# Optimization experiments

Measured on AMD Instinct MI355X. Metric: run time of the kernel, lower is better.

## Reference

```python
import jax, jax.numpy as jnp
import numpy as np

STATE_DIM = 512
N_AGENTS = 16
N_ACTIONS = 32
EMBED = 512          # mixing_embed_dim
Q_IN = STATE_DIM + N_AGENTS * N_ACTIONS  # 1024 (coma_critic arch)
ROWS = 32768         # bs * ts = 64 * 512


def _linear_params(key, d_in, d_out):
    kw, kb = jax.random.split(key)
    bound = 1.0 / np.sqrt(d_in)
    W = jax.random.uniform(kw, (d_in, d_out), minval=-bound, maxval=bound, dtype=jnp.float32)
    b = jax.random.uniform(kb, (d_out,), minval=-bound, maxval=bound, dtype=jnp.float32)
    return W, b


def setup_inputs() -> dict:
    key = jax.random.key(0)
    ks = jax.random.split(key, 8)
    states = jax.random.normal(ks[0], (ROWS, STATE_DIM), dtype=jnp.float32)
    actions = jax.random.uniform(ks[1], (ROWS, N_AGENTS * N_ACTIONS), dtype=jnp.float32)
    Qw1, Qb1 = _linear_params(ks[2], Q_IN, EMBED)
    Qw2, Qb2 = _linear_params(ks[3], EMBED, EMBED)
    Qw3, Qb3 = _linear_params(ks[4], EMBED, 1)
    Vw1, Vb1 = _linear_params(ks[5], STATE_DIM, EMBED)
    Vw2, Vb2 = _linear_params(ks[6], EMBED, EMBED)
    Vw3, Vb3 = _linear_params(ks[7], EMBED, 1)
    return {
        "states": states, "actions": actions,
        "Qw1": Qw1, "Qb1": Qb1, "Qw2": Qw2, "Qb2": Qb2, "Qw3": Qw3, "Qb3": Qb3,
        "Vw1": Vw1, "Vb1": Vb1, "Vw2": Vw2, "Vb2": Vb2, "Vw3": Vw3, "Vb3": Vb3,
    }


def _mlp3(x, W1, b1, W2, b2, W3, b3):
    h = jax.nn.relu(x @ W1 + b1)
    h = jax.nn.relu(h @ W2 + b2)
    return h @ W3 + b3


def reference(states, actions,
              Qw1, Qb1, Qw2, Qb2, Qw3, Qb3,
              Vw1, Vb1, Vw2, Vb2, Vw3, Vb3):
    # coma_critic arch: inputs = cat([states, joint-action one-hots], dim=1)
    inputs = jnp.concatenate([states, actions], axis=1)  # [bs*ts, Q_IN]
    q_outputs = _mlp3(inputs, Qw1, Qb1, Qw2, Qb2, Qw3, Qb3)  # [bs*ts, 1]
    v_outputs = _mlp3(states, Vw1, Vb1, Vw2, Vb2, Vw3, Vb3)  # [bs*ts, 1]
    return q_outputs, v_outputs
```

## Files before the change

kernel.cpp:

```cpp
#include <hip/hip_runtime.h>


#define ROWS 32768
#define EMBED 512

using frag_ab = __attribute__((ext_vector_type(8))) short;
using f32x4   = __attribute__((ext_vector_type(4))) float;

__device__ __forceinline__ unsigned short f2bf(float f) {
    unsigned int u = __builtin_bit_cast(unsigned int, f);
    return (unsigned short)((u + 0x7fffu + ((u >> 16) & 1u)) >> 16);
}

__device__ __forceinline__ unsigned pk2rne(float lo, float hi) {
    return (unsigned)f2bf(lo) | ((unsigned)f2bf(hi) << 16);
}

__device__ __forceinline__ void async_copy16(const void* g, void* l) {
    __builtin_amdgcn_global_load_lds(
        (const __attribute__((address_space(1))) unsigned int*)g,
        (__attribute__((address_space(3))) unsigned int*)l, 16, 0, 0);
}

#define VM8()   asm volatile("s_waitcnt vmcnt(8)" ::: "memory")
#define VM0()   asm volatile("s_waitcnt vmcnt(0)" ::: "memory")
#define SBAR()  __builtin_amdgcn_s_barrier()

__global__ __launch_bounds__(256)
void prep(const float* __restrict__ states, const float* __restrict__ actions,
          const float* __restrict__ Qw1, const float* __restrict__ Qw2,
          const float* __restrict__ Vw1, const float* __restrict__ Vw2,
          const float* __restrict__ qb3, const float* __restrict__ vb3,
          unsigned short* __restrict__ X,
          unsigned short* __restrict__ Qw1t, unsigned short* __restrict__ Qw2t,
          unsigned short* __restrict__ Vw1t, unsigned short* __restrict__ Vw2t,
          float* __restrict__ out) {
    const int b = blockIdx.x, tid = threadIdx.x;
    if (b < 16384) {
        int g = b * 256 + tid;
        int m = g >> 7, col = (g & 127) * 8;
        const float* src = (col < 512) ? states + (size_t)m * 512 + col
                                       : actions + (size_t)m * 512 + (col - 512);
        float4 f0 = ((const float4*)src)[0];
        float4 f1 = ((const float4*)src)[1];
        *(uint4*)(X + (size_t)m * 1024 + col) =
            make_uint4(pk2rne(f0.x, f0.y), pk2rne(f0.z, f0.w),
                       pk2rne(f1.x, f1.y), pk2rne(f1.z, f1.w));
    } else if (b < 16704) {
        __shared__ float T[64][65];
        int tg = b - 16384;
        const float* W; unsigned short* O; int Krows, kt, nt;
        if (tg < 128) { W = Qw1; O = Qw1t; Krows = 1024; kt = tg >> 3; nt = tg & 7; }
        else {
            tg -= 128; int seg = tg >> 6, r = tg & 63;
            kt = r >> 3; nt = r & 7; Krows = 512;
            W = (seg == 0) ? Qw2 : (seg == 1) ? Vw1 : Vw2;
            O = (seg == 0) ? Qw2t : (seg == 1) ? Vw1t : Vw2t;
        }
        const int k0 = kt * 64, n0 = nt * 64;
        const int rr = tid >> 4, c4 = (tid & 15) * 4;
#pragma unroll
        for (int p = 0; p < 4; ++p) {
            float4 v = *(const float4*)&W[(size_t)(k0 + p * 16 + rr) * 512 + n0 + c4];
            T[p * 16 + rr][c4]     = v.x;
            T[p * 16 + rr][c4 + 1] = v.y;
            T[p * 16 + rr][c4 + 2] = v.z;
            T[p * 16 + rr][c4 + 3] = v.w;
        }
        __syncthreads();
        const int n = tid >> 2, kc = (tid & 3) * 16;
        unsigned pk[8];
#pragma unroll
        for (int j = 0; j < 8; ++j)
            pk[j] = pk2rne(T[kc + 2 * j][n], T[kc + 2 * j + 1][n]);
        uint4* dst = (uint4*)(O + (size_t)(n0 + n) * Krows + k0 + kc);
        dst[0] = make_uint4(pk[0], pk[1], pk[2], pk[3]);
        dst[1] = make_uint4(pk[4], pk[5], pk[6], pk[7]);
    } else {
        int i = (b - 16704) * 256 + tid;
        out[i] = (i < ROWS) ? qb3[0] : vb3[0];
    }
}

__device__ __forceinline__ void gemm_256(
    const unsigned short* __restrict__ A, int ldaE,
    const unsigned short* __restrict__ Bt, int ldbE,
    int K, int bm, int bn, char* smb, f32x4 acc[8][4])
{
    const int tid = threadIdx.x, wave = tid >> 6, lane = tid & 63;
    const int im = wave >> 2, in = wave & 3;
    const int lrow = lane & 15, quad = lane >> 4;
    const int ldaB = ldaE * 2, ldbB = ldbE * 2;

    const int srow = wave * 8 + (lane >> 3);
    const int scol = (((lane & 7) ^ ((lane >> 3) & 7)) << 4);
    const char* gA = (const char*)A + (size_t)(bm + srow) * ldaB + scol;
    const char* gB = (const char*)Bt + (size_t)(bn + srow) * ldbB + scol;
    char* ldsAw = smb + wave * 1024;
    char* ldsBw = smb + 65536 + wave * 1024;

    auto stageTile = [&](int b) {
#pragma unroll
        for (int h = 0; h < 2; ++h) {
            const char* g = gA + (size_t)(h * 128) * ldaB;
            char* l = ldsAw + b * 32768 + h * 16384;
            async_copy16(g, l);
            async_copy16(g + (size_t)64 * ldaB, l + 8192);
        }
#pragma unroll
        for (int h = 0; h < 2; ++h) {
            const char* g = gB + (size_t)(h * 128) * ldbB;
            char* l = ldsBw + b * 32768 + h * 16384;
            async_copy16(g, l);
            async_copy16(g + (size_t)64 * ldbB, l + 8192);
        }
        gA += 128; gB += 128;
    };

    frag_ab a[4][2], b0[2][2], b1[2][2];

    auto readA = [&](int b, int mh) {
        const char* base = smb + b * 32768 + im * 16384;
#pragma unroll
        for (int i = 0; i < 4; ++i) {
            const int r = mh * 64 + i * 16 + lrow;
#pragma unroll
            for (int s = 0; s < 2; ++s)
                a[i][s] = *(const frag_ab*)(base + r * 128 +
                              (((s * 4 + quad) ^ (r & 7)) << 4));
        }
    };
    auto readB = [&](int b, int nh, frag_ab bb[2][2]) {
#pragma unroll
        for (int j = 0; j < 2; ++j) {
            const int nr = in * 64 + nh * 32 + j * 16 + lrow;
            const char* base = smb + 65536 + b * 32768 + (nr >> 7) * 16384;
            const int r = nr & 127;
#pragma unroll
            for (int s = 0; s < 2; ++s)
                bb[j][s] = *(const frag_ab*)(base + r * 128 +
                               (((s * 4 + quad) ^ (r & 7)) << 4));
        }
    };
    auto mma = [&](int mh, int nh, frag_ab bb[2][2]) {
        __builtin_amdgcn_s_setprio(1);
#pragma unroll
        for (int s = 0; s < 2; ++s)
#pragma unroll
            for (int i = 0; i < 4; ++i)
#pragma unroll
                for (int j = 0; j < 2; ++j)
                    acc[mh * 4 + i][nh * 2 + j] =
                        __builtin_amdgcn_mfma_f32_16x16x32_bf16(
                            a[i][s], bb[j][s], acc[mh * 4 + i][nh * 2 + j],
                            0, 0, 0);
        __builtin_amdgcn_s_setprio(0);
    };

    stageTile(0);
    stageTile(1);

    const int NT = K >> 6;
    int buf = 0;
    for (int t = 0; t < NT; ++t) {
        if (t + 1 < NT) VM8(); else VM0();
        SBAR();
        readA(buf, 0); readB(buf, 0, b0);
        mma(0, 0, b0);
        readB(buf, 1, b1);
        mma(0, 1, b1);
        readA(buf, 1);
        mma(1, 1, b1);
        mma(1, 0, b0);
        SBAR();
        if (t + 2 < NT) stageTile(buf);
        buf ^= 1;
    }
}

__device__ __forceinline__ void decode_work(int bid, int& mi, int& v) {
    int work = ((bid & 7) << 6) | (bid >> 3);
    mi = work >> 2; v = work & 3;
}

__global__ __launch_bounds__(512, 2)
void layer1(const unsigned short* __restrict__ X,
            const unsigned short* __restrict__ Qw1t,
            const unsigned short* __restrict__ Vw1t,
            const float* __restrict__ Qb1, const float* __restrict__ Vb1,
            unsigned short* __restrict__ h1Q, unsigned short* __restrict__ h1V) {
    __shared__ __align__(16) char smem[131072];
    int mi, v; decode_work(blockIdx.x, mi, v);
    const bool isV = v >= 2;
    const int bm = mi * 256, bn = (v & 1) * 256;
    const int K = isV ? 512 : 1024;
    const unsigned short* Wt = isV ? Vw1t : Qw1t;
    const float* bias = isV ? Vb1 : Qb1;
    unsigned short* H = isV ? h1V : h1Q;

    f32x4 acc[8][4] = {};
    gemm_256(X, 1024, Wt, K, K, bm, bn, smem, acc);

    const int tid = threadIdx.x, wave = tid >> 6, lane = tid & 63;
    const int im = wave >> 2, in = wave & 3;
    const int lrow = lane & 15, quad = lane >> 4;
#pragma unroll
    for (int j = 0; j < 4; ++j) {
        const int col = bn + in * 64 + j * 16 + lrow;
        const float bc = bias[col];
#pragma unroll
        for (int i = 0; i < 8; ++i) {
            const int row0 = bm + im * 128 + i * 16 + quad * 4;
#pragma unroll
            for (int r = 0; r < 4; ++r) {
                float val = acc[i][j][r] + bc;
                val = val > 0.0f ? val : 0.0f;
                H[(size_t)(row0 + r) * EMBED + col] = f2bf(val);
            }
        }
    }
}

__global__ __launch_bounds__(512, 2)
void layer2(const unsigned short* __restrict__ h1Q,
            const unsigned short* __restrict__ h1V,
            const unsigned short* __restrict__ Qw2t,
            const unsigned short* __restrict__ Vw2t,
            const float* __restrict__ Qb2, const float* __restrict__ Vb2,
            const float* __restrict__ Qw3, const float* __restrict__ Vw3,
            float* __restrict__ out) {
    __shared__ __align__(16) char smem[131072];
    int mi, v; decode_work(blockIdx.x, mi, v);
    const bool isV = v >= 2;
    const int bm = mi * 256, bn = (v & 1) * 256;
    const unsigned short* A  = isV ? h1V : h1Q;
    const unsigned short* Wt = isV ? Vw2t : Qw2t;
    const float* bias = isV ? Vb2 : Qb2;
    const float* w3   = isV ? Vw3 : Qw3;
    float* op = out + (isV ? ROWS : 0);

    f32x4 acc[8][4] = {};
    gemm_256(A, 512, Wt, 512, 512, bm, bn, smem, acc);

    const int tid = threadIdx.x, wave = tid >> 6, lane = tid & 63;
    const int im = wave >> 2, in = wave & 3;
    const int lrow = lane & 15, quad = lane >> 4;
    float bc[4], wc[4];
#pragma unroll
    for (int j = 0; j < 4; ++j) {
        const int col = bn + in * 64 + j * 16 + lrow;
        bc[j] = bias[col];
        wc[j] = w3[col];
    }
#pragma unroll
    for (int i = 0; i < 8; ++i) {
#pragma unroll
        for (int r = 0; r < 4; ++r) {
            float s = 0.0f;
#pragma unroll
            for (int j = 0; j < 4; ++j) {
                float val = acc[i][j][r] + bc[j];
                val = val > 0.0f ? val : 0.0f;
                s += val * wc[j];
            }
#pragma unroll
            for (int m = 1; m < 16; m <<= 1) s += __shfl_xor(s, m, 64);
            if (lrow == 0)
                atomicAdd(&op[bm + im * 128 + i * 16 + quad * 4 + r], s);
        }
    }
}

extern "C" void kernel_launch(void* const* d_in, const int* in_sizes, int n_in,
                              void* d_out, int out_size, void* d_ws, size_t ws_size,
                              hipStream_t stream) {
    const float* states  = (const float*)d_in[0];
    const float* actions = (const float*)d_in[1];
    const float* Qw1 = (const float*)d_in[2];
    const float* Qb1 = (const float*)d_in[3];
    const float* Qw2 = (const float*)d_in[4];
    const float* Qb2 = (const float*)d_in[5];
    const float* Qw3 = (const float*)d_in[6];
    const float* Qb3 = (const float*)d_in[7];
    const float* Vw1 = (const float*)d_in[8];
    const float* Vb1 = (const float*)d_in[9];
    const float* Vw2 = (const float*)d_in[10];
    const float* Vb2 = (const float*)d_in[11];
    const float* Vw3 = (const float*)d_in[12];
    const float* Vb3 = (const float*)d_in[13];
    float* out = (float*)d_out;

    char* ws = (char*)d_ws;
    unsigned short* X    = (unsigned short*)ws;
    unsigned short* h1Q  = (unsigned short*)(ws + 67108864);
    unsigned short* h1V  = (unsigned short*)(ws + 100663296);
    unsigned short* Qw1t = (unsigned short*)(ws + 134217728);
    unsigned short* Qw2t = Qw1t + 512 * 1024;
    unsigned short* Vw1t = Qw2t + 512 * 512;
    unsigned short* Vw2t = Vw1t + 512 * 512;

    prep<<<dim3(16960), dim3(256), 0, stream>>>(states, actions, Qw1, Qw2, Vw1, Vw2,
                                                Qb3, Vb3, X, Qw1t, Qw2t, Vw1t, Vw2t, out);

    layer1<<<dim3(512), dim3(512), 0, stream>>>(X, Qw1t, Vw1t, Qb1, Vb1, h1Q, h1V);
    layer2<<<dim3(512), dim3(512), 0, stream>>>(h1Q, h1V, Qw2t, Vw2t, Qb2, Vb2, Qw3, Vw3, out);
}
```

Measured before the change: 283.0 us.

## Fuse fp32-to-bf16 input conversion into layer1 and merge Q/V work per block

Drops the separate prep pass that converted states/actions to a bf16 X buffer. layer1 now loads fp32 A tiles into registers, converts them to bf16 and writes them to LDS while B tiles stream in asynchronously. Each block handles the Q and V GEMMs for the same row tile back to back, so grids shrink to 256 blocks and the states tile is reread while likely still in cache. This removes a 64MB round-trip through memory, at the cost of register-staged A loads, extra LDS waits and half as many blocks for parallelism.

After: 292.1 us. 1.03x slower.

```diff
diff --git a/kernel.cpp b/kernel.cpp
--- a/kernel.cpp
+++ b/kernel.cpp
@@ -22,33 +22,23 @@
         (__attribute__((address_space(3))) unsigned int*)l, 16, 0, 0);
 }
 
+#define VM12()  asm volatile("s_waitcnt vmcnt(12)" ::: "memory")
 #define VM8()   asm volatile("s_waitcnt vmcnt(8)" ::: "memory")
 #define VM0()   asm volatile("s_waitcnt vmcnt(0)" ::: "memory")
+#define LGKM0() asm volatile("s_waitcnt lgkmcnt(0)" ::: "memory")
 #define SBAR()  __builtin_amdgcn_s_barrier()
 
 __global__ __launch_bounds__(256)
-void prep(const float* __restrict__ states, const float* __restrict__ actions,
-          const float* __restrict__ Qw1, const float* __restrict__ Qw2,
+void prep(const float* __restrict__ Qw1, const float* __restrict__ Qw2,
           const float* __restrict__ Vw1, const float* __restrict__ Vw2,
           const float* __restrict__ qb3, const float* __restrict__ vb3,
-          unsigned short* __restrict__ X,
           unsigned short* __restrict__ Qw1t, unsigned short* __restrict__ Qw2t,
           unsigned short* __restrict__ Vw1t, unsigned short* __restrict__ Vw2t,
           float* __restrict__ out) {
     const int b = blockIdx.x, tid = threadIdx.x;
-    if (b < 16384) {
-        int g = b * 256 + tid;
-        int m = g >> 7, col = (g & 127) * 8;
-        const float* src = (col < 512) ? states + (size_t)m * 512 + col
-                                       : actions + (size_t)m * 512 + (col - 512);
-        float4 f0 = ((const float4*)src)[0];
-        float4 f1 = ((const float4*)src)[1];
-        *(uint4*)(X + (size_t)m * 1024 + col) =
-            make_uint4(pk2rne(f0.x, f0.y), pk2rne(f0.z, f0.w),
-                       pk2rne(f1.x, f1.y), pk2rne(f1.z, f1.w));
-    } else if (b < 16704) {
+    if (b < 320) {
         __shared__ float T[64][65];
-        int tg = b - 16384;
+        int tg = b;
         const float* W; unsigned short* O; int Krows, kt, nt;
         if (tg < 128) { W = Qw1; O = Qw1t; Krows = 1024; kt = tg >> 3; nt = tg & 7; }
         else {
@@ -77,42 +67,198 @@
         dst[0] = make_uint4(pk[0], pk[1], pk[2], pk[3]);
         dst[1] = make_uint4(pk[4], pk[5], pk[6], pk[7]);
     } else {
-        int i = (b - 16704) * 256 + tid;
+        int i = (b - 320) * 256 + tid;
         out[i] = (i < ROWS) ? qb3[0] : vb3[0];
     }
 }
 
+__device__ __forceinline__ void decode_work(int bid, int& mi, int& n) {
+    int work = ((bid & 7) << 5) | (bid >> 3);
+    mi = work >> 1; n = work & 1;
+}
+
+__global__ __launch_bounds__(512, 2)
+void layer1(const float* __restrict__ states, const float* __restrict__ actions,
+            const unsigned short* __restrict__ Qw1t,
+            const unsigned short* __restrict__ Vw1t,
+            const float* __restrict__ Qb1, const float* __restrict__ Vb1,
+            unsigned short* __restrict__ h1Q, unsigned short* __restrict__ h1V) {
+    __shared__ __align__(16) char smem[131072];
+    const int tid = threadIdx.x, wave = tid >> 6, lane = tid & 63;
+    int mi, nh; decode_work(blockIdx.x, mi, nh);
+    const int bm = mi * 256, bn = nh * 256;
+    const int im = wave >> 2, in = wave & 3;
+    const int lrow = lane & 15, quad = lane >> 4;
+
+    const int arow = wave * 8 + (lane >> 3);
+    const int acol = (lane & 7) * 8;
+    const size_t aOff = (size_t)(bm + arow) * 512 + acol;
+
+    const int srow = wave * 8 + (lane >> 3);
+    const int scol = (((lane & 7) ^ ((lane >> 3) & 7)) << 4);
+
+    float4 rA[4][2];
+    frag_ab a[4][2], b0[2][2], b1[2][2];
+    f32x4 acc[8][4] = {};
+
+    auto loadA = [&](const float* p) {
+#pragma unroll
+        for (int q = 0; q < 4; ++q) {
+            const float* s = p + (size_t)(64 * q) * 512;
+            rA[q][0] = *(const float4*)s;
+            rA[q][1] = *(const float4*)(s + 4);
+        }
+    };
+    auto writeA = [&](int b) {
+#pragma unroll
+        for (int q = 0; q < 4; ++q) {
+            const int R = arow + 64 * q, half = R >> 7, r = R & 127;
+            const int c = (lane & 7) ^ (r & 7);
+            *(uint4*)(smem + b * 32768 + half * 16384 + r * 128 + (c << 4)) =
+                make_uint4(pk2rne(rA[q][0].x, rA[q][0].y),
+                           pk2rne(rA[q][0].z, rA[q][0].w),
+                           pk2rne(rA[q][1].x, rA[q][1].y),
+                           pk2rne(rA[q][1].z, rA[q][1].w));
+        }
+    };
+    auto readA = [&](int b, int mh) {
+        const char* base = smem + b * 32768 + im * 16384;
+#pragma unroll
+        for (int i = 0; i < 4; ++i) {
+            const int r = mh * 64 + i * 16 + lrow;
+#pragma unroll
+            for (int s = 0; s < 2; ++s)
+                a[i][s] = *(const frag_ab*)(base + r * 128 +
+                              (((s * 4 + quad) ^ (r & 7)) << 4));
+        }
+    };
+    auto readB = [&](int b, int nhh, frag_ab bb[2][2]) {
+#pragma unroll
+        for (int j = 0; j < 2; ++j) {
+            const int nr = in * 64 + nhh * 32 + j * 16 + lrow;
+            const char* base = smem + 65536 + b * 32768 + (nr >> 7) * 16384;
+            const int r = nr & 127;
+#pragma unroll
+            for (int s = 0; s < 2; ++s)
+                bb[j][s] = *(const frag_ab*)(base + r * 128 +
+                               (((s * 4 + quad) ^ (r & 7)) << 4));
+        }
+    };
+    auto mma = [&](int mh, int nhh, frag_ab bb[2][2]) {
+        __builtin_amdgcn_s_setprio(1);
+#pragma unroll
+        for (int s = 0; s < 2; ++s)
+#pragma unroll
+            for (int i = 0; i < 4; ++i)
+#pragma unroll
+                for (int j = 0; j < 2; ++j)
+                    acc[mh * 4 + i][nhh * 2 + j] =
+                        __builtin_amdgcn_mfma_f32_16x16x32_bf16(
+                            a[i][s], bb[j][s], acc[mh * 4 + i][nhh * 2 + j],
+                            0, 0, 0);
+        __builtin_amdgcn_s_setprio(0);
+    };
+
+    auto run = [&](const float* aP0, const float* aP1, int nt0, int nt1,
+                   const unsigned short* Wt, int ldbE) {
+        const int NT = nt0 + nt1;
+        const int ldbB = ldbE * 2;
+        const char* gB = (const char*)Wt + (size_t)(bn + srow) * ldbB + scol;
+        auto stageB = [&](int b) {
+#pragma unroll
+            for (int h = 0; h < 2; ++h) {
+                const char* g = gB + (size_t)(h * 128) * ldbB;
+                char* l = smem + 65536 + wave * 1024 + b * 32768 + h * 16384;
+                async_copy16(g, l);
+                async_copy16(g + (size_t)64 * ldbB, l + 8192);
+            }
+            gB += 128;
+        };
+        auto aTile = [&](int kt) {
+            return (kt < nt0) ? aP0 + aOff + kt * 64
+                              : aP1 + aOff + (kt - nt0) * 64;
+        };
+        loadA(aTile(0));
+        stageB(0);
+        writeA(0);
+        LGKM0();
+        for (int t = 0; t < NT; ++t) {
+            const bool more = t + 1 < NT;
+            if (more) { loadA(aTile(t + 1)); stageB((t + 1) & 1); }
+            if (more) VM12(); else VM0();
+            SBAR();
+            const int bb = t & 1;
+            readA(bb, 0); readB(bb, 0, b0);
+            mma(0, 0, b0);
+            readB(bb, 1, b1);
+            mma(0, 1, b1);
+            readA(bb, 1);
+            mma(1, 1, b1);
+            mma(1, 0, b0);
+            if (more) writeA((t + 1) & 1);
+            LGKM0();
+            SBAR();
+        }
+    };
+
+    auto epilogue = [&](const float* bias, unsigned short* H) {
+#pragma unroll
+        for (int j = 0; j < 4; ++j) {
+            const int col = bn + in * 64 + j * 16 + lrow;
+            const float bc = bias[col];
+#pragma unroll
+            for (int i = 0; i < 8; ++i) {
+                const int row0 = bm + im * 128 + i * 16 + quad * 4;
+#pragma unroll
+                for (int r = 0; r < 4; ++r) {
+                    float val = acc[i][j][r] + bc;
+                    val = val > 0.0f ? val : 0.0f;
+                    H[(size_t)(row0 + r) * EMBED + col] = f2bf(val);
+                }
+            }
+        }
+    };
+
+    run(states, actions, 8, 8, Qw1t, 1024);
+    epilogue(Qb1, h1Q);
+#pragma unroll
+    for (int i = 0; i < 8; ++i)
+#pragma unroll
+        for (int j = 0; j < 4; ++j) acc[i][j] = f32x4{0.f, 0.f, 0.f, 0.f};
+    run(states, states, 8, 0, Vw1t, 512);
+    epilogue(Vb1, h1V);
+}
+
 __device__ __forceinline__ void gemm_256(
-    const unsigned short* __restrict__ A, int ldaE,
-    const unsigned short* __restrict__ Bt, int ldbE,
-    int K, int bm, int bn, char* smb, f32x4 acc[8][4])
+    const unsigned short* __restrict__ A,
+    const unsigned short* __restrict__ Bt,
+    int bm, int bn, char* smb, f32x4 acc[8][4])
 {
     const int tid = threadIdx.x, wave = tid >> 6, lane = tid & 63;
     const int im = wave >> 2, in = wave & 3;
     const int lrow = lane & 15, quad = lane >> 4;
-    const int ldaB = ldaE * 2, ldbB = ldbE * 2;
 
     const int srow = wave * 8 + (lane >> 3);
     const int scol = (((lane & 7) ^ ((lane >> 3) & 7)) << 4);
-    const char* gA = (const char*)A + (size_t)(bm + srow) * ldaB + scol;
-    const char* gB = (const char*)Bt + (size_t)(bn + srow) * ldbB + scol;
+    const char* gA = (const char*)A + (size_t)(bm + srow) * 1024 + scol;
+    const char* gB = (const char*)Bt + (size_t)(bn + srow) * 1024 + scol;
     char* ldsAw = smb + wave * 1024;
     char* ldsBw = smb + 65536 + wave * 1024;
 
     auto stageTile = [&](int b) {
 #pragma unroll
         for (int h = 0; h < 2; ++h) {
-            const char* g = gA + (size_t)(h * 128) * ldaB;
+            const char* g = gA + (size_t)(h * 128) * 1024;
             char* l = ldsAw + b * 32768 + h * 16384;
             async_copy16(g, l);
-            async_copy16(g + (size_t)64 * ldaB, l + 8192);
+            async_copy16(g + (size_t)64 * 1024, l + 8192);
         }
 #pragma unroll
         for (int h = 0; h < 2; ++h) {
-            const char* g = gB + (size_t)(h * 128) * ldbB;
+            const char* g = gB + (size_t)(h * 128) * 1024;
             char* l = ldsBw + b * 32768 + h * 16384;
             async_copy16(g, l);
-            async_copy16(g + (size_t)64 * ldbB, l + 8192);
+            async_copy16(g + (size_t)64 * 1024, l + 8192);
         }
         gA += 128; gB += 128;
     };
@@ -160,7 +306,7 @@
     stageTile(0);
     stageTile(1);
 
-    const int NT = K >> 6;
+    const int NT = 8;
     int buf = 0;
     for (int t = 0; t < NT; ++t) {
         if (t + 1 < NT) VM8(); else VM0();
@@ -178,49 +324,6 @@
     }
 }
 
-__device__ __forceinline__ void decode_work(int bid, int& mi, int& v) {
-    int work = ((bid & 7) << 6) | (bid >> 3);
-    mi = work >> 2; v = work & 3;
-}
-
-__global__ __launch_bounds__(512, 2)
-void layer1(const unsigned short* __restrict__ X,
-            const unsigned short* __restrict__ Qw1t,
-            const unsigned short* __restrict__ Vw1t,
-            const float* __restrict__ Qb1, const float* __restrict__ Vb1,
-            unsigned short* __restrict__ h1Q, unsigned short* __restrict__ h1V) {
-    __shared__ __align__(16) char smem[131072];
-    int mi, v; decode_work(blockIdx.x, mi, v);
-    const bool isV = v >= 2;
-    const int bm = mi * 256, bn = (v & 1) * 256;
-    const int K = isV ? 512 : 1024;
-    const unsigned short* Wt = isV ? Vw1t : Qw1t;
-    const float* bias = isV ? Vb1 : Qb1;
-    unsigned short* H = isV ? h1V : h1Q;
-
-    f32x4 acc[8][4] = {};
-    gemm_256(X, 1024, Wt, K, K, bm, bn, smem, acc);
-
-    const int tid = threadIdx.x, wave = tid >> 6, lane = tid & 63;
-    const int im = wave >> 2, in = wave & 3;
-    const int lrow = lane & 15, quad = lane >> 4;
-#pragma unroll
-    for (int j = 0; j < 4; ++j) {
-        const int col = bn + in * 64 + j * 16 + lrow;
-        const float bc = bias[col];
-#pragma unroll
-        for (int i = 0; i < 8; ++i) {
-            const int row0 = bm + im * 128 + i * 16 + quad * 4;
-#pragma unroll
-            for (int r = 0; r < 4; ++r) {
-                float val = acc[i][j][r] + bc;
-                val = val > 0.0f ? val : 0.0f;
-                H[(size_t)(row0 + r) * EMBED + col] = f2bf(val);
-            }
-        }
-    }
-}
-
 __global__ __launch_bounds__(512, 2)
 void layer2(const unsigned short* __restrict__ h1Q,
             const unsigned short* __restrict__ h1V,
@@ -230,45 +333,49 @@
             const float* __restrict__ Qw3, const float* __restrict__ Vw3,
             float* __restrict__ out) {
     __shared__ __align__(16) char smem[131072];
-    int mi, v; decode_work(blockIdx.x, mi, v);
-    const bool isV = v >= 2;
-    const int bm = mi * 256, bn = (v & 1) * 256;
-    const unsigned short* A  = isV ? h1V : h1Q;
-    const unsigned short* Wt = isV ? Vw2t : Qw2t;
-    const float* bias = isV ? Vb2 : Qb2;
-    const float* w3   = isV ? Vw3 : Qw3;
-    float* op = out + (isV ? ROWS : 0);
-
-    f32x4 acc[8][4] = {};
-    gemm_256(A, 512, Wt, 512, 512, bm, bn, smem, acc);
-
     const int tid = threadIdx.x, wave = tid >> 6, lane = tid & 63;
+    int mi, nh; decode_work(blockIdx.x, mi, nh);
+    const int bm = mi * 256, bn = nh * 256;
     const int im = wave >> 2, in = wave & 3;
     const int lrow = lane & 15, quad = lane >> 4;
-    float bc[4], wc[4];
-#pragma unroll
-    for (int j = 0; j < 4; ++j) {
-        const int col = bn + in * 64 + j * 16 + lrow;
-        bc[j] = bias[col];
-        wc[j] = w3[col];
-    }
-#pragma unroll
-    for (int i = 0; i < 8; ++i) {
-#pragma unroll
-        for (int r = 0; r < 4; ++r) {
-            float s = 0.0f;
-#pragma unroll
-            for (int j = 0; j < 4; ++j) {
-                float val = acc[i][j][r] + bc[j];
-                val = val > 0.0f ? val : 0.0f;
-                s += val * wc[j];
+
+    f32x4 acc[8][4] = {};
+
+    auto epilogue = [&](const float* bias, const float* w3, float* op) {
+        float bc[4], wc[4];
+#pragma unroll
+        for (int j = 0; j < 4; ++j) {
+            const int col = bn + in * 64 + j * 16 + lrow;
+            bc[j] = bias[col];
+            wc[j] = w3[col];
+        }
+#pragma unroll
+        for (int i = 0; i < 8; ++i) {
+#pragma unroll
+            for (int r = 0; r < 4; ++r) {
+                float s = 0.0f;
+#pragma unroll
+                for (int j = 0; j < 4; ++j) {
+                    float val = acc[i][j][r] + bc[j];
+                    val = val > 0.0f ? val : 0.0f;
+                    s += val * wc[j];
+                }
+#pragma unroll
+                for (int m = 1; m < 16; m <<= 1) s += __shfl_xor(s, m, 64);
+                if (lrow == 0)
+                    atomicAdd(&op[bm + im * 128 + i * 16 + quad * 4 + r], s);
             }
-#pragma unroll
-            for (int m = 1; m < 16; m <<= 1) s += __shfl_xor(s, m, 64);
-            if (lrow == 0)
-                atomicAdd(&op[bm + im * 128 + i * 16 + quad * 4 + r], s);
-        }
-    }
+        }
+    };
+
+    gemm_256(h1Q, Qw2t, bm, bn, smem, acc);
+    epilogue(Qb2, Qw3, out);
+#pragma unroll
+    for (int i = 0; i < 8; ++i)
+#pragma unroll
+        for (int j = 0; j < 4; ++j) acc[i][j] = f32x4{0.f, 0.f, 0.f, 0.f};
+    gemm_256(h1V, Vw2t, bm, bn, smem, acc);
+    epilogue(Vb2, Vw3, out + ROWS);
 }
 
 extern "C" void kernel_launch(void* const* d_in, const int* in_sizes, int n_in,
@@ -291,17 +398,18 @@
     float* out = (float*)d_out;
 
     char* ws = (char*)d_ws;
-    unsigned short* X    = (unsigned short*)ws;
-    unsigned short* h1Q  = (unsigned short*)(ws + 67108864);
-    unsigned short* h1V  = (unsigned short*)(ws + 100663296);
-    unsigned short* Qw1t = (unsigned short*)(ws + 134217728);
+    unsigned short* h1Q  = (unsigned short*)ws;
+    unsigned short* h1V  = (unsigned short*)(ws + 33554432);
+    unsigned short* Qw1t = (unsigned short*)(ws + 67108864);
     unsigned short* Qw2t = Qw1t + 512 * 1024;
     unsigned short* Vw1t = Qw2t + 512 * 512;
     unsigned short* Vw2t = Vw1t + 512 * 512;
 
-    prep<<<dim3(16960), dim3(256), 0, stream>>>(states, actions, Qw1, Qw2, Vw1, Vw2,
-                                                Qb3, Vb3, X, Qw1t, Qw2t, Vw1t, Vw2t, out);
-
-    layer1<<<dim3(512), dim3(512), 0, stream>>>(X, Qw1t, Vw1t, Qb1, Vb1, h1Q, h1V);
-    layer2<<<dim3(512), dim3(512), 0, stream>>>(h1Q, h1V, Qw2t, Vw2t, Qb2, Vb2, Qw3, Vw3, out);
-}
+    prep<<<dim3(576), dim3(256), 0, stream>>>(Qw1, Qw2, Vw1, Vw2, Qb3, Vb3,
+                                              Qw1t, Qw2t, Vw1t, Vw2t, out);
+
+    layer1<<<dim3(256), dim3(512), 0, stream>>>(states, actions, Qw1t, Vw1t,
+                                                Qb1, Vb1, h1Q, h1V);
+    layer2<<<dim3(256), dim3(512), 0, stream>>>(h1Q, h1V, Qw2t, Vw2t,
+                                                Qb2, Vb2, Qw3, Vw3, out);
+}
```

## Switch GEMM mainloop to K=32 tiles with four-stage async pipeline

Applied to the files above, without the earlier changes.

Replaces the two-buffer K=64 tile GEMM with a K=32 step, four-slot ring buffer that keeps three tiles in flight. It issues the next prefetch before computing the current tile, which removes the second barrier per iteration. The new LDS layout drops the XOR swizzle, and the block-to-work mapping changes so that all Q blocks come first, then all V blocks. Smaller K steps mean more barriers and less MFMA work per barrier, and the unswizzled 64-byte rows may cause LDS bank conflicts.

After: 299.1 us. 1.06x slower.

```diff
diff --git a/kernel.cpp b/kernel.cpp
--- a/kernel.cpp
+++ b/kernel.cpp
@@ -23,6 +23,7 @@
 }
 
 #define VM8()   asm volatile("s_waitcnt vmcnt(8)" ::: "memory")
+#define VM4()   asm volatile("s_waitcnt vmcnt(4)" ::: "memory")
 #define VM0()   asm volatile("s_waitcnt vmcnt(0)" ::: "memory")
 #define SBAR()  __builtin_amdgcn_s_barrier()
 
@@ -82,105 +83,72 @@
     }
 }
 
-__device__ __forceinline__ void gemm_256(
+__device__ __forceinline__ void gemm_k32(
     const unsigned short* __restrict__ A, int ldaE,
     const unsigned short* __restrict__ Bt, int ldbE,
-    int K, int bm, int bn, char* smb, f32x4 acc[8][4])
+    int NT, int bm, int bn, char* smb, f32x4 acc[8][4])
 {
     const int tid = threadIdx.x, wave = tid >> 6, lane = tid & 63;
     const int im = wave >> 2, in = wave & 3;
     const int lrow = lane & 15, quad = lane >> 4;
-    const int ldaB = ldaE * 2, ldbB = ldbE * 2;
-
-    const int srow = wave * 8 + (lane >> 3);
-    const int scol = (((lane & 7) ^ ((lane >> 3) & 7)) << 4);
-    const char* gA = (const char*)A + (size_t)(bm + srow) * ldaB + scol;
-    const char* gB = (const char*)Bt + (size_t)(bn + srow) * ldbB + scol;
-    char* ldsAw = smb + wave * 1024;
-    char* ldsBw = smb + 65536 + wave * 1024;
-
-    auto stageTile = [&](int b) {
-#pragma unroll
-        for (int h = 0; h < 2; ++h) {
-            const char* g = gA + (size_t)(h * 128) * ldaB;
-            char* l = ldsAw + b * 32768 + h * 16384;
-            async_copy16(g, l);
-            async_copy16(g + (size_t)64 * ldaB, l + 8192);
-        }
-#pragma unroll
-        for (int h = 0; h < 2; ++h) {
-            const char* g = gB + (size_t)(h * 128) * ldbB;
-            char* l = ldsBw + b * 32768 + h * 16384;
-            async_copy16(g, l);
-            async_copy16(g + (size_t)64 * ldbB, l + 8192);
-        }
-        gA += 128; gB += 128;
+    const size_t ldaB = (size_t)ldaE * 2, ldbB = (size_t)ldbE * 2;
+
+    const int srow = wave * 32 + (lane >> 2);
+    const int sk   = (lane & 3) * 16;
+    const char* gA = (const char*)A + (size_t)(bm + srow) * ldaB + sk;
+    const char* gB = (const char*)Bt + (size_t)(bn + srow) * ldbB + sk;
+    char* ldsAw = smb + wave * 2048;
+    char* ldsBw = smb + 65536 + wave * 2048;
+
+    auto stage = [&](int t) {
+        const int b = t & 3;
+        const char* a  = gA + (size_t)t * 64;
+        const char* bs = gB + (size_t)t * 64;
+        async_copy16(a,             ldsAw + b * 16384);
+        async_copy16(a + 16 * ldaB, ldsAw + b * 16384 + 1024);
+        async_copy16(bs,             ldsBw + b * 16384);
+        async_copy16(bs + 16 * ldbB, ldsBw + b * 16384 + 1024);
     };
 
-    frag_ab a[4][2], b0[2][2], b1[2][2];
-
-    auto readA = [&](int b, int mh) {
-        const char* base = smb + b * 32768 + im * 16384;
-#pragma unroll
-        for (int i = 0; i < 4; ++i) {
-            const int r = mh * 64 + i * 16 + lrow;
-#pragma unroll
-            for (int s = 0; s < 2; ++s)
-                a[i][s] = *(const frag_ab*)(base + r * 128 +
-                              (((s * 4 + quad) ^ (r & 7)) << 4));
-        }
-    };
-    auto readB = [&](int b, int nh, frag_ab bb[2][2]) {
-#pragma unroll
-        for (int j = 0; j < 2; ++j) {
-            const int nr = in * 64 + nh * 32 + j * 16 + lrow;
-            const char* base = smb + 65536 + b * 32768 + (nr >> 7) * 16384;
-            const int r = nr & 127;
-#pragma unroll
-            for (int s = 0; s < 2; ++s)
-                bb[j][s] = *(const frag_ab*)(base + r * 128 +
-                               (((s * 4 + quad) ^ (r & 7)) << 4));
-        }
-    };
-    auto mma = [&](int mh, int nh, frag_ab bb[2][2]) {
+    auto compute = [&](int t) {
+        const char* baseA = smb + (t & 3) * 16384 + im * 8192;
+        const char* baseB = smb + 65536 + (t & 3) * 16384 + in * 4096;
+        frag_ab a[8], b[4];
+#pragma unroll
+        for (int i = 0; i < 8; ++i)
+            a[i] = *(const frag_ab*)(baseA + (i * 16 + lrow) * 64 + quad * 16);
+#pragma unroll
+        for (int j = 0; j < 4; ++j)
+            b[j] = *(const frag_ab*)(baseB + (j * 16 + lrow) * 64 + quad * 16);
         __builtin_amdgcn_s_setprio(1);
 #pragma unroll
-        for (int s = 0; s < 2; ++s)
-#pragma unroll
-            for (int i = 0; i < 4; ++i)
-#pragma unroll
-                for (int j = 0; j < 2; ++j)
-                    acc[mh * 4 + i][nh * 2 + j] =
-                        __builtin_amdgcn_mfma_f32_16x16x32_bf16(
-                            a[i][s], bb[j][s], acc[mh * 4 + i][nh * 2 + j],
-                            0, 0, 0);
+        for (int i = 0; i < 8; ++i)
+#pragma unroll
+            for (int j = 0; j < 4; ++j)
+                acc[i][j] = __builtin_amdgcn_mfma_f32_16x16x32_bf16(
+                    a[i], b[j], acc[i][j], 0, 0, 0);
         __builtin_amdgcn_s_setprio(0);
     };
 
-    stageTile(0);
-    stageTile(1);
-
-    const int NT = K >> 6;
-    int buf = 0;
+    stage(0);
+    if (NT > 1) stage(1);
+    if (NT > 2) stage(2);
+
     for (int t = 0; t < NT; ++t) {
-        if (t + 1 < NT) VM8(); else VM0();
+        if (t + 3 <= NT) VM8();
+        else if (t + 2 <= NT) VM4();
+        else VM0();
         SBAR();
-        readA(buf, 0); readB(buf, 0, b0);
-        mma(0, 0, b0);
-        readB(buf, 1, b1);
-        mma(0, 1, b1);
-        readA(buf, 1);
-        mma(1, 1, b1);
-        mma(1, 0, b0);
-        SBAR();
-        if (t + 2 < NT) stageTile(buf);
-        buf ^= 1;
-    }
-}
-
-__device__ __forceinline__ void decode_work(int bid, int& mi, int& v) {
-    int work = ((bid & 7) << 6) | (bid >> 3);
-    mi = work >> 2; v = work & 3;
+        if (t + 3 < NT) stage(t + 3);
+        compute(t);
+    }
+}
+
+__device__ __forceinline__ void decode_work(int bid, bool& isV, int& mi, int& nh) {
+    isV = bid >= 256;
+    int r = bid & 255;
+    int work = ((r & 7) << 5) | (r >> 3);
+    mi = work >> 1; nh = work & 1;
 }
 
 __global__ __launch_bounds__(512, 2)
@@ -190,16 +158,16 @@
             const float* __restrict__ Qb1, const float* __restrict__ Vb1,
             unsigned short* __restrict__ h1Q, unsigned short* __restrict__ h1V) {
     __shared__ __align__(16) char smem[131072];
-    int mi, v; decode_work(blockIdx.x, mi, v);
-    const bool isV = v >= 2;
-    const int bm = mi * 256, bn = (v & 1) * 256;
-    const int K = isV ? 512 : 1024;
+    bool isV; int mi, nh; decode_work(blockIdx.x, isV, mi, nh);
+    const int bm = mi * 256, bn = nh * 256;
+    const int NT = isV ? 16 : 32;
     const unsigned short* Wt = isV ? Vw1t : Qw1t;
+    const int ldb = isV ? 512 : 1024;
     const float* bias = isV ? Vb1 : Qb1;
     unsigned short* H = isV ? h1V : h1Q;
 
     f32x4 acc[8][4] = {};
-    gemm_256(X, 1024, Wt, K, K, bm, bn, smem, acc);
+    gemm_k32(X, 1024, Wt, ldb, NT, bm, bn, smem, acc);
 
     const int tid = threadIdx.x, wave = tid >> 6, lane = tid & 63;
     const int im = wave >> 2, in = wave & 3;
@@ -230,9 +198,8 @@
             const float* __restrict__ Qw3, const float* __restrict__ Vw3,
             float* __restrict__ out) {
     __shared__ __align__(16) char smem[131072];
-    int mi, v; decode_work(blockIdx.x, mi, v);
-    const bool isV = v >= 2;
-    const int bm = mi * 256, bn = (v & 1) * 256;
+    bool isV; int mi, nh; decode_work(blockIdx.x, isV, mi, nh);
+    const int bm = mi * 256, bn = nh * 256;
     const unsigned short* A  = isV ? h1V : h1Q;
     const unsigned short* Wt = isV ? Vw2t : Qw2t;
     const float* bias = isV ? Vb2 : Qb2;
@@ -240,7 +207,7 @@
     float* op = out + (isV ? ROWS : 0);
 
     f32x4 acc[8][4] = {};
-    gemm_256(A, 512, Wt, 512, 512, bm, bn, smem, acc);
+    gemm_k32(A, 512, Wt, 512, 16, bm, bn, smem, acc);
 
     const int tid = threadIdx.x, wave = tid >> 6, lane = tid & 63;
     const int im = wave >> 2, in = wave & 3;
```
